# Performance work log

Measured on AMD Instinct MI355X. Metric: run time of the kernel, lower is better.

The kernel has to match this reference:

```python
import jax, jax.numpy as jnp
import numpy as np

GROUPS = 32
EPS = 1e-3  # keras GroupNormalization default epsilon


def setup_inputs() -> dict:
    key = jax.random.key(0)
    ks = jax.random.split(key, 7)
    B, H, W, C = 16, 32, 32, 512
    inputs = jax.random.normal(ks[0], (B, H, W, C), dtype=jnp.float32)
    gamma = jnp.ones((C,), dtype=jnp.float32)
    beta = jnp.zeros((C,), dtype=jnp.float32)
    # EinsumDense 'bhwc,cae->bhwae', output last dims (C,3), bias axes 'ae'
    W_qkv = jax.random.normal(ks[1], (C, C, 3), dtype=jnp.float32) / np.sqrt(C)
    b_qkv = jnp.zeros((C, 3), dtype=jnp.float32)
    # EinsumDense 'bhwc,cd->bhwd', bias axes 'd'
    W_out = jax.random.normal(ks[2], (C, C), dtype=jnp.float32) / np.sqrt(C)
    b_out = jnp.zeros((C,), dtype=jnp.float32)
    return {
        "inputs": inputs,
        "gamma": gamma,
        "beta": beta,
        "W_qkv": W_qkv,
        "b_qkv": b_qkv,
        "W_out": W_out,
        "b_out": b_out,
    }


def group_norm(x, gamma, beta):
    B, H, W, C = x.shape
    g = GROUPS
    xr = x.reshape(B, H, W, g, C // g)
    mean = jnp.mean(xr, axis=(1, 2, 4), keepdims=True)
    var = jnp.var(xr, axis=(1, 2, 4), keepdims=True)
    xn = (xr - mean) * jax.lax.rsqrt(var + EPS)
    return xn.reshape(B, H, W, C) * gamma + beta


def reference(inputs, gamma, beta, W_qkv, b_qkv, W_out, b_out):
    B, H, W, C = inputs.shape
    scale = C ** (-0.5)
    x = group_norm(inputs, gamma, beta)
    # QKV projection: bhwc,cae->bhwae  (+ bias over 'ae')
    qkv = jnp.einsum("bhwc,cae->bhwae", x, W_qkv) + b_qkv
    q, k, v = qkv[..., 0], qkv[..., 1], qkv[..., 2]  # each [B,H,W,C]
    # full spatial attention: [B,H,W,H,W]
    attn = jnp.einsum("bhwc,btlc->bhwtl", q, k) * scale
    attn = attn.reshape(B, H, W, H * W)
    attn = jax.nn.softmax(attn, axis=-1)
    attn = attn.reshape(B, H, W, H, W)
    out = jnp.einsum("bhwtl,btlc->bhwc", attn, v)
    out = jnp.einsum("bhwc,cd->bhwd", out, W_out) + b_out
    return inputs + out
```

## Files before the change

### kernel.cpp

```cpp
#include <hip/hip_runtime.h>
#include <hip/hip_bf16.h>

#define NB    16
#define SP    1024
#define NC    512
#define NG    32
#define MTOT  (NB*SP)
#define EPSV  1e-3f
#define SCALE 0.04419417382415922f

using f32x4   = __attribute__((ext_vector_type(4))) float;
using short8  = __attribute__((ext_vector_type(8))) short;
using short4v = __attribute__((ext_vector_type(4))) short;
using bf16x8v = __attribute__((ext_vector_type(8))) __bf16;

__device__ __forceinline__ unsigned short f2bf(float f) {
  union { float f; unsigned int u; } x; x.f = f;
  unsigned int u = x.u;
  unsigned int r = (u + 0x7FFFu + ((u >> 16) & 1u)) >> 16;
  return (unsigned short)r;
}
__device__ __forceinline__ float bf2f(unsigned short b) {
  union { unsigned int u; float f; } x; x.u = ((unsigned int)b) << 16;
  return x.f;
}

#define GLOAD_LDS16(g, l)                                                     \
  __builtin_amdgcn_global_load_lds(                                           \
      (const __attribute__((address_space(1))) void*)(g),                     \
      (__attribute__((address_space(3))) void*)(l), 16, 0, 0)

__global__ __launch_bounds__(256) void gn_stats_k(const float* __restrict__ x,
                                                  float2* __restrict__ stats) {
  int bg = blockIdx.x;
  int b = bg >> 5, g = bg & 31;
  int tid = threadIdx.x;
  int c = tid & 15, s0 = tid >> 4;
  const float* base = x + (long)b * SP * NC + g * 16 + c;
  float s = 0.f, ss = 0.f;
  for (int sp = s0; sp < SP; sp += 16) {
    float v = base[(long)sp * NC];
    s += v; ss += v * v;
  }
  for (int o = 32; o > 0; o >>= 1) { s += __shfl_xor(s, o); ss += __shfl_xor(ss, o); }
  __shared__ float rs[4], rss[4];
  int lane = tid & 63, wv = tid >> 6;
  if (lane == 0) { rs[wv] = s; rss[wv] = ss; }
  __syncthreads();
  if (tid == 0) {
    float S = rs[0] + rs[1] + rs[2] + rs[3];
    float SS = rss[0] + rss[1] + rss[2] + rss[3];
    float mean = S * (1.f / 16384.f);
    float var  = SS * (1.f / 16384.f) - mean * mean;
    stats[bg] = make_float2(mean, rsqrtf(var + EPSV));
  }
}

__global__ __launch_bounds__(256) void gn_apply_k(const float* __restrict__ x,
                                                  const float2* __restrict__ stats,
                                                  const float* __restrict__ gamma,
                                                  const float* __restrict__ beta,
                                                  unsigned short* __restrict__ xn) {
  long t = (long)blockIdx.x * 256 + threadIdx.x;
  long base = t * 8;
  int c = (int)(base & 511);
  int b = (int)(base >> 19);
  float2 st = stats[b * NG + (c >> 4)];
  f32x4 v0 = *reinterpret_cast<const f32x4*>(x + base);
  f32x4 v1 = *reinterpret_cast<const f32x4*>(x + base + 4);
  f32x4 g0 = *reinterpret_cast<const f32x4*>(gamma + c);
  f32x4 g1 = *reinterpret_cast<const f32x4*>(gamma + c + 4);
  f32x4 b0 = *reinterpret_cast<const f32x4*>(beta + c);
  f32x4 b1 = *reinterpret_cast<const f32x4*>(beta + c + 4);
  short8 o;
  #pragma unroll
  for (int q = 0; q < 4; ++q) {
    float sc = st.y * g0[q];
    o[q] = (short)f2bf(v0[q] * sc + (b0[q] - st.x * sc));
  }
  #pragma unroll
  for (int q = 0; q < 4; ++q) {
    float sc = st.y * g1[q];
    o[q + 4] = (short)f2bf(v1[q] * sc + (b1[q] - st.x * sc));
  }
  *reinterpret_cast<short8*>(xn + base) = o;
}

__global__ __launch_bounds__(256) void pack_wqkv_k(const float* __restrict__ W,
                                                   const float* __restrict__ bq,
                                                   unsigned short* __restrict__ Wp,
                                                   float* __restrict__ bp) {
  int idx = blockIdx.x * 256 + threadIdx.x;
  int n = idx >> 9, c = idx & 511;
  int e = n >> 9, a = n & 511;
  Wp[idx] = f2bf(W[((long)c * 512 + a) * 3 + e]);
  if (idx < 1536) {
    int e2 = idx >> 9, a2 = idx & 511;
    bp[idx] = bq[a2 * 3 + e2];
  }
}

__global__ __launch_bounds__(256) void pack_wout_k(const float* __restrict__ W,
                                                   unsigned short* __restrict__ Wp) {
  int idx = blockIdx.x * 256 + threadIdx.x;
  int n = idx >> 9, c = idx & 511;
  Wp[idx] = f2bf(W[(long)c * 512 + n]);
}

__global__ void transpose_v_k(const unsigned short* __restrict__ qkv,
                              unsigned short* __restrict__ vT) {
  __shared__ unsigned short t[32][33];
  int bs = blockIdx.x, bc = blockIdx.y, b = blockIdx.z;
  int tx = threadIdx.x, ty = threadIdx.y;
  #pragma unroll
  for (int k = 0; k < 4; ++k) {
    int s = bs * 32 + ty + k * 8, c = bc * 32 + tx;
    t[ty + k * 8][tx] = qkv[((long)b * SP + s) * 1536 + 1024 + c];
  }
  __syncthreads();
  #pragma unroll
  for (int k = 0; k < 4; ++k) {
    int c = bc * 32 + ty + k * 8, s = bs * 32 + tx;
    vT[((long)b * NC + c) * SP + s] = t[tx][ty + k * 8];
  }
}

__global__ __launch_bounds__(256) void softmax_k(unsigned short* __restrict__ S) {
  long row = blockIdx.x;
  unsigned short* r = S + row * 1024;
  int tid = threadIdx.x, lane = tid & 63, wv = tid >> 6;
  short4v raw = *reinterpret_cast<const short4v*>(r + tid * 4);
  float v[4];
  #pragma unroll
  for (int q = 0; q < 4; ++q) v[q] = bf2f((unsigned short)raw[q]);
  float m = fmaxf(fmaxf(v[0], v[1]), fmaxf(v[2], v[3]));
  for (int o = 32; o > 0; o >>= 1) m = fmaxf(m, __shfl_xor(m, o));
  __shared__ float wm[4], ws[4];
  if (lane == 0) wm[wv] = m;
  __syncthreads();
  float rmax = fmaxf(fmaxf(wm[0], wm[1]), fmaxf(wm[2], wm[3]));
  float e[4]; float ssum = 0.f;
  #pragma unroll
  for (int q = 0; q < 4; ++q) { e[q] = __expf(v[q] - rmax); ssum += e[q]; }
  for (int o = 32; o > 0; o >>= 1) ssum += __shfl_xor(ssum, o);
  if (lane == 0) ws[wv] = ssum;
  __syncthreads();
  float inv = 1.f / (ws[0] + ws[1] + ws[2] + ws[3]);
  short4v pv;
  #pragma unroll
  for (int q = 0; q < 4; ++q) pv[q] = (short)f2bf(e[q] * inv);
  *reinterpret_cast<short4v*>(r + tid * 4) = pv;
}

template <int EPI>
__global__ __launch_bounds__(512, 2) void gemm256(
    const unsigned short* __restrict__ Ap, long strideA, int lda,
    const unsigned short* __restrict__ Bp, long strideB, int ldb,
    unsigned short* __restrict__ Op, long strideO, int ldo,
    const float* __restrict__ bias, int K, float scale) {
  constexpr int SLOT = 32768;
  extern __shared__ unsigned char smem[];
  const int tid = threadIdx.x;
  const int lane = tid & 63, wv = tid >> 6;
  const int wm2 = wv >> 2, wn4 = wv & 3;

  const int nwg  = gridDim.x * gridDim.y;
  const int flat = blockIdx.y * gridDim.x + blockIdx.x;
  const int w    = (flat & 7) * (nwg >> 3) + (flat >> 3);
  const int bn = (w % gridDim.x) * 256;
  const int bm = (w / gridDim.x) * 256;
  const int z = blockIdx.z;
  const unsigned short* Ag = Ap + (long)z * strideA;
  const unsigned short* Bg = Bp + (long)z * strideB;

  long offA0, offA1, offB0, offB1;
  { int sid = tid, sr = sid >> 3, sl = (sid & 7) ^ (sr & 7);
    offA0 = (long)(bm + sr * 2 + (sl >> 2)) * lda + (sl & 3) * 8;
    offB0 = (long)(bn + sr * 2 + (sl >> 2)) * ldb + (sl & 3) * 8;
    sid = 512 + tid; sr = sid >> 3; sl = (sid & 7) ^ (sr & 7);
    offA1 = (long)(bm + sr * 2 + (sl >> 2)) * lda + (sl & 3) * 8;
    offB1 = (long)(bn + sr * 2 + (sl >> 2)) * ldb + (sl & 3) * 8; }
  const int ldsA0 = wv * 1024;
  const int ldsA1 = 8192  + wv * 1024;
  const int ldsB0 = 16384 + wv * 1024;
  const int ldsB1 = 24576 + wv * 1024;

  int aoff[8], boff[4];
  #pragma unroll
  for (int i = 0; i < 8; ++i) {
    int r = wm2 * 128 + i * 16 + (lane & 15);
    int sr = r >> 1, sl = ((r & 1) * 4 + (lane >> 4)) ^ (sr & 7);
    aoff[i] = sr * 128 + sl * 16;
  }
  #pragma unroll
  for (int j = 0; j < 4; ++j) {
    int r = wn4 * 64 + j * 16 + (lane & 15);
    int sr = r >> 1, sl = ((r & 1) * 4 + (lane >> 4)) ^ (sr & 7);
    boff[j] = 16384 + sr * 128 + sl * 16;
  }

#define STAGE6(tt, sb) do { long kt = (long)(tt) * 32;                \
    GLOAD_LDS16(Ag + offA0 + kt, smem + (sb) + ldsA0);                \
    GLOAD_LDS16(Ag + offA1 + kt, smem + (sb) + ldsA1);                \
    GLOAD_LDS16(Bg + offB0 + kt, smem + (sb) + ldsB0);                \
    GLOAD_LDS16(Bg + offB1 + kt, smem + (sb) + ldsB1); } while (0)

#define READS6(av, bv, sa) do {                                       \
    _Pragma("unroll")                                                 \
    for (int i = 0; i < 8; ++i)                                       \
      av[i] = *reinterpret_cast<const short8*>((sa) + aoff[i]);       \
    _Pragma("unroll")                                                 \
    for (int j = 0; j < 4; ++j)                                       \
      bv[j] = *reinterpret_cast<const short8*>((sa) + boff[j]); } while (0)

#define MFMA32(av, bv) do {                                           \
    _Pragma("unroll")                                                 \
    for (int i = 0; i < 8; ++i)                                       \
      _Pragma("unroll")                                               \
      for (int j = 0; j < 4; ++j)                                     \
        acc[i][j] = __builtin_amdgcn_mfma_f32_16x16x32_bf16(          \
            __builtin_bit_cast(bf16x8v, av[i]),                       \
            __builtin_bit_cast(bf16x8v, bv[j]), acc[i][j], 0, 0, 0);  \
    } while (0)

  const int NT = K >> 5;
  #pragma unroll
  for (int t = 0; t < 3; ++t)
    STAGE6(t, t * SLOT);
  asm volatile("s_waitcnt vmcnt(4)" ::: "memory");
  __builtin_amdgcn_s_barrier();
  __builtin_amdgcn_sched_barrier(0);

  short8 a0[8], b0[4], a1[8], b1[4];
  READS6(a0, b0, smem);
  f32x4 acc[8][4] = {};

  for (int t = 0; t < NT; t += 2) {
    if (t + 3 < NT) STAGE6(t + 3, ((t + 3) & 3) * SLOT);
    if (t + 1 < NT) { const unsigned char* sa = smem + ((t + 1) & 3) * SLOT; READS6(a1, b1, sa); }
    __builtin_amdgcn_sched_barrier(0);
    __builtin_amdgcn_s_setprio(1);
    MFMA32(a0, b0);
    __builtin_amdgcn_s_setprio(0);
    __builtin_amdgcn_sched_barrier(0);
    if (t + 3 < NT) asm volatile("s_waitcnt vmcnt(4)" ::: "memory");
    else            asm volatile("s_waitcnt vmcnt(0)" ::: "memory");
    __builtin_amdgcn_s_barrier();
    __builtin_amdgcn_sched_barrier(0);

    if (t + 1 < NT) {
      if (t + 4 < NT) STAGE6(t + 4, ((t + 4) & 3) * SLOT);
      if (t + 2 < NT) { const unsigned char* sa = smem + ((t + 2) & 3) * SLOT; READS6(a0, b0, sa); }
      __builtin_amdgcn_sched_barrier(0);
      __builtin_amdgcn_s_setprio(1);
      MFMA32(a1, b1);
      __builtin_amdgcn_s_setprio(0);
      __builtin_amdgcn_sched_barrier(0);
      if (t + 4 < NT) asm volatile("s_waitcnt vmcnt(4)" ::: "memory");
      else            asm volatile("s_waitcnt vmcnt(0)" ::: "memory");
      __builtin_amdgcn_s_barrier();
      __builtin_amdgcn_sched_barrier(0);
    }
  }
#undef STAGE6
#undef READS6
#undef MFMA32

  const int colb = bn + wn4 * 64 + (lane & 15);
  const int rowb = bm + wm2 * 128 + (lane >> 4) * 4;
  #pragma unroll
  for (int i = 0; i < 8; ++i) {
    #pragma unroll
    for (int r = 0; r < 4; ++r) {
      long rowg = rowb + i * 16 + r;
      #pragma unroll
      for (int j = 0; j < 4; ++j) {
        int colg = colb + j * 16;
        float v = acc[i][j][r];
        if (EPI == 0) {
          v += bias[colg];
          Op[(long)z * strideO + rowg * ldo + colg] = f2bf(v);
        } else {
          Op[(long)z * strideO + rowg * ldo + colg] = f2bf(v * scale);
        }
      }
    }
  }
}

template <int EPI>
__global__ __launch_bounds__(512, 2) void gemm8(
    const unsigned short* __restrict__ Ap, long strideA, int lda,
    const unsigned short* __restrict__ Bp, long strideB, int ldb,
    void* __restrict__ Op, long strideO, int ldo,
    const float* __restrict__ bias, const float* __restrict__ residual,
    int K, float scale) {
  constexpr int SLOT = 24576;
  extern __shared__ unsigned char smem[];
  const int tid = threadIdx.x;
  const int lane = tid & 63, wv = tid >> 6;
  const int wm2 = wv >> 2, wn4 = wv & 3;

  const int nwg  = gridDim.x * gridDim.y;
  const int flat = blockIdx.y * gridDim.x + blockIdx.x;
  const int w    = (flat & 7) * (nwg >> 3) + (flat >> 3);
  const int bn = (w % gridDim.x) * 256;
  const int bm = (w / gridDim.x) * 128;
  const int z = blockIdx.z;
  const unsigned short* Ag = Ap + (long)z * strideA;
  const unsigned short* Bg = Bp + (long)z * strideB;

  long offA;
  { int sid = tid, sr = sid >> 3, sl = (sid & 7) ^ (sr & 7);
    offA = (long)(bm + sr * 2 + (sl >> 2)) * lda + (sl & 3) * 8; }
  long offB0, offB1;
  { int sid = tid, sr = sid >> 3, sl = (sid & 7) ^ (sr & 7);
    offB0 = (long)(bn + sr * 2 + (sl >> 2)) * ldb + (sl & 3) * 8;
    sid = 512 + tid; sr = sid >> 3; sl = (sid & 7) ^ (sr & 7);
    offB1 = (long)(bn + sr * 2 + (sl >> 2)) * ldb + (sl & 3) * 8; }
  const int ldsA_off  = wv * 1024;
  const int ldsB0_off = 8192 + wv * 1024;
  const int ldsB1_off = 16384 + wv * 1024;

  int aoff[4], boff[4];
  #pragma unroll
  for (int i = 0; i < 4; ++i) {
    int r = wm2 * 64 + i * 16 + (lane & 15);
    int sr = r >> 1, sl = ((r & 1) * 4 + (lane >> 4)) ^ (sr & 7);
    aoff[i] = sr * 128 + sl * 16;
  }
  #pragma unroll
  for (int j = 0; j < 4; ++j) {
    int r = wn4 * 64 + j * 16 + (lane & 15);
    int sr = r >> 1, sl = ((r & 1) * 4 + (lane >> 4)) ^ (sr & 7);
    boff[j] = 8192 + sr * 128 + sl * 16;
  }

#define STAGE(tt, sb) do { long kt = (long)(tt) * 32;                 \
    GLOAD_LDS16(Ag + offA + kt,  smem + (sb) + ldsA_off);             \
    GLOAD_LDS16(Bg + offB0 + kt, smem + (sb) + ldsB0_off);            \
    GLOAD_LDS16(Bg + offB1 + kt, smem + (sb) + ldsB1_off); } while (0)

#define READS(av, bv, sa) do {                                        \
    _Pragma("unroll")                                                 \
    for (int i = 0; i < 4; ++i)                                       \
      av[i] = *reinterpret_cast<const short8*>((sa) + aoff[i]);       \
    _Pragma("unroll")                                                 \
    for (int j = 0; j < 4; ++j)                                       \
      bv[j] = *reinterpret_cast<const short8*>((sa) + boff[j]); } while (0)

#define MFMA16(av, bv) do {                                           \
    _Pragma("unroll")                                                 \
    for (int i = 0; i < 4; ++i)                                       \
      _Pragma("unroll")                                               \
      for (int j = 0; j < 4; ++j)                                     \
        acc[i][j] = __builtin_amdgcn_mfma_f32_16x16x32_bf16(          \
            __builtin_bit_cast(bf16x8v, av[i]),                       \
            __builtin_bit_cast(bf16x8v, bv[j]), acc[i][j], 0, 0, 0);  \
    } while (0)

  const int NT = K >> 5;
  #pragma unroll
  for (int t = 0; t < 3; ++t)
    if (t < NT) STAGE(t, t * SLOT);
  asm volatile("s_waitcnt vmcnt(3)" ::: "memory");
  __builtin_amdgcn_s_barrier();
  __builtin_amdgcn_sched_barrier(0);

  short8 a0[4], b0[4], a1[4], b1[4];
  READS(a0, b0, smem);
  f32x4 acc[4][4] = {};

  for (int t = 0; t < NT; t += 2) {
    if (t + 3 < NT) STAGE(t + 3, ((t + 3) & 3) * SLOT);
    if (t + 1 < NT) { const unsigned char* sa = smem + ((t + 1) & 3) * SLOT; READS(a1, b1, sa); }
    __builtin_amdgcn_sched_barrier(0);
    __builtin_amdgcn_s_setprio(1);
    MFMA16(a0, b0);
    __builtin_amdgcn_s_setprio(0);
    __builtin_amdgcn_sched_barrier(0);
    if (t + 3 < NT) asm volatile("s_waitcnt vmcnt(3)" ::: "memory");
    else            asm volatile("s_waitcnt vmcnt(0)" ::: "memory");
    __builtin_amdgcn_s_barrier();
    __builtin_amdgcn_sched_barrier(0);

    if (t + 1 < NT) {
      if (t + 4 < NT) STAGE(t + 4, ((t + 4) & 3) * SLOT);
      if (t + 2 < NT) { const unsigned char* sa = smem + ((t + 2) & 3) * SLOT; READS(a0, b0, sa); }
      __builtin_amdgcn_sched_barrier(0);
      __builtin_amdgcn_s_setprio(1);
      MFMA16(a1, b1);
      __builtin_amdgcn_s_setprio(0);
      __builtin_amdgcn_sched_barrier(0);
      if (t + 4 < NT) asm volatile("s_waitcnt vmcnt(3)" ::: "memory");
      else            asm volatile("s_waitcnt vmcnt(0)" ::: "memory");
      __builtin_amdgcn_s_barrier();
      __builtin_amdgcn_sched_barrier(0);
    }
  }
#undef STAGE
#undef READS
#undef MFMA16

  const int colb = bn + wn4 * 64 + (lane & 15);
  const int rowb = bm + wm2 * 64 + (lane >> 4) * 4;
  #pragma unroll
  for (int i = 0; i < 4; ++i) {
    #pragma unroll
    for (int r = 0; r < 4; ++r) {
      int rowg = rowb + i * 16 + r;
      #pragma unroll
      for (int j = 0; j < 4; ++j) {
        int colg = colb + j * 16;
        float v = acc[i][j][r];
        if (EPI == 2) {
          ((unsigned short*)Op)[(long)z * strideO + (long)rowg * ldo + colg] = f2bf(v * scale);
        } else {
          v += bias[colg] + residual[(long)rowg * ldo + colg];
          ((float*)Op)[(long)rowg * ldo + colg] = v;
        }
      }
    }
  }
}

extern "C" void kernel_launch(void* const* d_in, const int* in_sizes, int n_in,
                              void* d_out, int out_size, void* d_ws, size_t ws_size,
                              hipStream_t stream) {
  const float* x     = (const float*)d_in[0];
  const float* gamma = (const float*)d_in[1];
  const float* beta  = (const float*)d_in[2];
  const float* Wqkv  = (const float*)d_in[3];
  const float* bqkv  = (const float*)d_in[4];
  const float* Wout  = (const float*)d_in[5];
  const float* bout  = (const float*)d_in[6];
  float* out = (float*)d_out;

  char* ws = (char*)d_ws;
  float2*         stats = (float2*)(ws + 0);
  unsigned short* wqkvP = (unsigned short*)(ws + 4096);
  float*          bqP   = (float*)(ws + 1576960);
  unsigned short* woutT = (unsigned short*)(ws + 1583104);
  unsigned short* qkv   = (unsigned short*)(ws + 2107392);
  unsigned short* vT    = (unsigned short*)(ws + 52439040);
  unsigned short* Sbuf  = (unsigned short*)(ws + 69216256);
  unsigned short* attn  = (unsigned short*)(ws + 136325120);
  unsigned short* xn    = (unsigned short*)(ws + 153102336);

  (void)hipFuncSetAttribute((const void*)gemm256<0>,
        hipFuncAttributeMaxDynamicSharedMemorySize, 131072);
  (void)hipFuncSetAttribute((const void*)gemm256<2>,
        hipFuncAttributeMaxDynamicSharedMemorySize, 131072);
  (void)hipFuncSetAttribute((const void*)gemm8<2>,
        hipFuncAttributeMaxDynamicSharedMemorySize, 98304);
  (void)hipFuncSetAttribute((const void*)gemm8<3>,
        hipFuncAttributeMaxDynamicSharedMemorySize, 98304);

  gn_stats_k<<<512, 256, 0, stream>>>(x, stats);
  gn_apply_k<<<4096, 256, 0, stream>>>(x, stats, gamma, beta, xn);
  pack_wqkv_k<<<3072, 256, 0, stream>>>(Wqkv, bqkv, wqkvP, bqP);
  pack_wout_k<<<1024, 256, 0, stream>>>(Wout, woutT);

  gemm256<0><<<dim3(6, 64, 1), 512, 131072, stream>>>(
      xn, 0L, NC, wqkvP, 0L, NC, qkv, 0L, 1536,
      bqP, NC, 1.f);

  transpose_v_k<<<dim3(32, 16, 16), dim3(32, 8), 0, stream>>>(qkv, vT);

  gemm256<2><<<dim3(4, 4, 16), 512, 131072, stream>>>(
      qkv, (long)SP * 1536, 1536, qkv + 512, (long)SP * 1536, 1536,
      Sbuf, (long)SP * SP, SP, nullptr, NC, SCALE);

  softmax_k<<<MTOT, 256, 0, stream>>>(Sbuf);

  gemm8<2><<<dim3(2, 8, 16), 512, 98304, stream>>>(
      Sbuf, (long)SP * SP, SP, vT, (long)NC * SP, SP,
      attn, (long)SP * NC, NC, nullptr, nullptr, SP, 1.f);

  gemm8<3><<<dim3(2, 128, 1), 512, 98304, stream>>>(
      attn, 0L, NC, woutT, 0L, NC, out, 0L, NC,
      bout, x, NC, 1.f);
}
```

Baseline: 273.0 us.

## Restructure gemm256 main loop into interleaved 4-phase load/compute pipeline

```diff
diff --git a/kernel.cpp b/kernel.cpp
--- a/kernel.cpp
+++ b/kernel.cpp
@@ -153,7 +153,7 @@
 }
 
 template <int EPI>
-__global__ __launch_bounds__(512, 2) void gemm256(
+__global__ __launch_bounds__(512, 2) void gemm256p(
     const unsigned short* __restrict__ Ap, long strideA, int lda,
     const unsigned short* __restrict__ Bp, long strideB, int ldb,
     unsigned short* __restrict__ Op, long strideO, int ldo,
@@ -199,72 +199,64 @@
     boff[j] = 16384 + sr * 128 + sl * 16;
   }
 
-#define STAGE6(tt, sb) do { long kt = (long)(tt) * 32;                \
+#define STAGE4(tt, sb) do { long kt = (long)(tt) * 32;                \
     GLOAD_LDS16(Ag + offA0 + kt, smem + (sb) + ldsA0);                \
     GLOAD_LDS16(Ag + offA1 + kt, smem + (sb) + ldsA1);                \
     GLOAD_LDS16(Bg + offB0 + kt, smem + (sb) + ldsB0);                \
     GLOAD_LDS16(Bg + offB1 + kt, smem + (sb) + ldsB1); } while (0)
 
-#define READS6(av, bv, sa) do {                                       \
-    _Pragma("unroll")                                                 \
-    for (int i = 0; i < 8; ++i)                                       \
-      av[i] = *reinterpret_cast<const short8*>((sa) + aoff[i]);       \
-    _Pragma("unroll")                                                 \
-    for (int j = 0; j < 4; ++j)                                       \
-      bv[j] = *reinterpret_cast<const short8*>((sa) + boff[j]); } while (0)
-
-#define MFMA32(av, bv) do {                                           \
-    _Pragma("unroll")                                                 \
-    for (int i = 0; i < 8; ++i)                                       \
-      _Pragma("unroll")                                               \
-      for (int j = 0; j < 4; ++j)                                     \
-        acc[i][j] = __builtin_amdgcn_mfma_f32_16x16x32_bf16(          \
-            __builtin_bit_cast(bf16x8v, av[i]),                       \
-            __builtin_bit_cast(bf16x8v, bv[j]), acc[i][j], 0, 0, 0);  \
-    } while (0)
-
   const int NT = K >> 5;
-  #pragma unroll
-  for (int t = 0; t < 3; ++t)
-    STAGE6(t, t * SLOT);
+  STAGE4(0, 0);
+  STAGE4(1, SLOT);
   asm volatile("s_waitcnt vmcnt(4)" ::: "memory");
   __builtin_amdgcn_s_barrier();
-  __builtin_amdgcn_sched_barrier(0);
-
-  short8 a0[8], b0[4], a1[8], b1[4];
-  READS6(a0, b0, smem);
+
   f32x4 acc[8][4] = {};
-
-  for (int t = 0; t < NT; t += 2) {
-    if (t + 3 < NT) STAGE6(t + 3, ((t + 3) & 3) * SLOT);
-    if (t + 1 < NT) { const unsigned char* sa = smem + ((t + 1) & 3) * SLOT; READS6(a1, b1, sa); }
-    __builtin_amdgcn_sched_barrier(0);
-    __builtin_amdgcn_s_setprio(1);
-    MFMA32(a0, b0);
-    __builtin_amdgcn_s_setprio(0);
-    __builtin_amdgcn_sched_barrier(0);
-    if (t + 3 < NT) asm volatile("s_waitcnt vmcnt(4)" ::: "memory");
-    else            asm volatile("s_waitcnt vmcnt(0)" ::: "memory");
-    __builtin_amdgcn_s_barrier();
-    __builtin_amdgcn_sched_barrier(0);
-
-    if (t + 1 < NT) {
-      if (t + 4 < NT) STAGE6(t + 4, ((t + 4) & 3) * SLOT);
-      if (t + 2 < NT) { const unsigned char* sa = smem + ((t + 2) & 3) * SLOT; READS6(a0, b0, sa); }
+  for (int t = 0; t < NT; ++t) {
+    const unsigned char* sa = smem + (t & 3) * SLOT;
+    const int t2 = t + 2;
+    const bool st = (t2 < NT);
+    const int sb = (t2 & 3) * SLOT;
+    const long kt2 = (long)t2 * 32;
+    short8 bfr[4];
+    #pragma unroll
+    for (int q = 0; q < 4; ++q) {
+      short8 av0 = *reinterpret_cast<const short8*>(sa + aoff[2 * q]);
+      short8 av1 = *reinterpret_cast<const short8*>(sa + aoff[2 * q + 1]);
+      if (q == 0) {
+        #pragma unroll
+        for (int j = 0; j < 4; ++j)
+          bfr[j] = *reinterpret_cast<const short8*>(sa + boff[j]);
+      }
+      if (st) {
+        if (q == 0) GLOAD_LDS16(Ag + offA0 + kt2, smem + sb + ldsA0);
+        if (q == 1) GLOAD_LDS16(Ag + offA1 + kt2, smem + sb + ldsA1);
+        if (q == 2) GLOAD_LDS16(Bg + offB0 + kt2, smem + sb + ldsB0);
+        if (q == 3) GLOAD_LDS16(Bg + offB1 + kt2, smem + sb + ldsB1);
+      }
+      __builtin_amdgcn_s_barrier();
+      asm volatile("s_waitcnt lgkmcnt(0)" ::: "memory");
       __builtin_amdgcn_sched_barrier(0);
       __builtin_amdgcn_s_setprio(1);
-      MFMA32(a1, b1);
+      #pragma unroll
+      for (int j = 0; j < 4; ++j) {
+        acc[2 * q][j] = __builtin_amdgcn_mfma_f32_16x16x32_bf16(
+            __builtin_bit_cast(bf16x8v, av0),
+            __builtin_bit_cast(bf16x8v, bfr[j]), acc[2 * q][j], 0, 0, 0);
+        acc[2 * q + 1][j] = __builtin_amdgcn_mfma_f32_16x16x32_bf16(
+            __builtin_bit_cast(bf16x8v, av1),
+            __builtin_bit_cast(bf16x8v, bfr[j]), acc[2 * q + 1][j], 0, 0, 0);
+      }
       __builtin_amdgcn_s_setprio(0);
       __builtin_amdgcn_sched_barrier(0);
-      if (t + 4 < NT) asm volatile("s_waitcnt vmcnt(4)" ::: "memory");
-      else            asm volatile("s_waitcnt vmcnt(0)" ::: "memory");
+      if (q == 3) {
+        if (st)              asm volatile("s_waitcnt vmcnt(4)" ::: "memory");
+        else if (t + 1 < NT) asm volatile("s_waitcnt vmcnt(0)" ::: "memory");
+      }
       __builtin_amdgcn_s_barrier();
-      __builtin_amdgcn_sched_barrier(0);
     }
   }
-#undef STAGE6
-#undef READS6
-#undef MFMA32
+#undef STAGE4
 
   const int colb = bn + wn4 * 64 + (lane & 15);
   const int rowb = bm + wm2 * 128 + (lane >> 4) * 4;
@@ -447,9 +439,9 @@
   unsigned short* attn  = (unsigned short*)(ws + 136325120);
   unsigned short* xn    = (unsigned short*)(ws + 153102336);
 
-  (void)hipFuncSetAttribute((const void*)gemm256<0>,
+  (void)hipFuncSetAttribute((const void*)gemm256p<0>,
         hipFuncAttributeMaxDynamicSharedMemorySize, 131072);
-  (void)hipFuncSetAttribute((const void*)gemm256<2>,
+  (void)hipFuncSetAttribute((const void*)gemm256p<2>,
         hipFuncAttributeMaxDynamicSharedMemorySize, 131072);
   (void)hipFuncSetAttribute((const void*)gemm8<2>,
         hipFuncAttributeMaxDynamicSharedMemorySize, 98304);
@@ -461,13 +453,13 @@
   pack_wqkv_k<<<3072, 256, 0, stream>>>(Wqkv, bqkv, wqkvP, bqP);
   pack_wout_k<<<1024, 256, 0, stream>>>(Wout, woutT);
 
-  gemm256<0><<<dim3(6, 64, 1), 512, 131072, stream>>>(
+  gemm256p<0><<<dim3(6, 64, 1), 512, 131072, stream>>>(
       xn, 0L, NC, wqkvP, 0L, NC, qkv, 0L, 1536,
       bqP, NC, 1.f);
 
   transpose_v_k<<<dim3(32, 16, 16), dim3(32, 8), 0, stream>>>(qkv, vT);
 
-  gemm256<2><<<dim3(4, 4, 16), 512, 131072, stream>>>(
+  gemm256p<2><<<dim3(4, 4, 16), 512, 131072, stream>>>(
       qkv, (long)SP * 1536, 1536, qkv + 512, (long)SP * 1536, 1536,
       Sbuf, (long)SP * SP, SP, nullptr, NC, SCALE);
 
```

After: 270.6 us. Within noise of the previous version (-0.9%).
